# Kernel optimization log

Measured on AMD Instinct MI355X. Metric: run time of the kernel, lower is better.

## Reference

```python
import jax, jax.numpy as jnp
from jax import lax
import numpy as np

T, B, I, H, F, KEEP = 1000, 512, 64, 64, 128, 5
ALPHA = 20.0 / 100.0  # dt / tau


def setup_inputs() -> dict:
    key = jax.random.key(0)
    ks = jax.random.split(key, 9)
    s = 1.0 / np.sqrt(H)
    return {
        "x": jax.random.normal(ks[0], (T, B, I), jnp.float32),
        "h0": jnp.zeros((B, H), jnp.float32),
        "W_in": jax.random.normal(ks[1], (H, I), jnp.float32) * s,
        "b_in": jax.random.normal(ks[2], (H,), jnp.float32) * s,
        "W_hh": jax.random.normal(ks[3], (H, H), jnp.float32) * s,
        "b_hh": jax.random.normal(ks[4], (H,), jnp.float32) * s,
        "W1": jax.random.normal(ks[5], (F, KEEP * H), jnp.float32) / np.sqrt(KEEP * H),
        "b1": jax.random.normal(ks[6], (F,), jnp.float32) * 0.01,
        "W2": jax.random.normal(ks[7], (H, F), jnp.float32) / np.sqrt(F),
        "b2": jax.random.normal(ks[8], (H,), jnp.float32) * 0.01,
    }


def reference(x, h0, W_in, b_in, W_hh, b_hh, W1, b1, W2, b2):
    # CT-RNN with leaky integration; feedback via MLP on the last 5 hiddens
    # once 5 steps have accumulated. KC = 0.5*I, so the feedback mix is
    # h = 0.5*h_obs + 0.5*h_mlp.
    Tn, Bn, _ = x.shape
    Hn = h0.shape[1]
    buf0 = jnp.zeros((KEEP, Bn, Hn), x.dtype)  # oldest-first ring of hiddens

    def step(carry, inp):
        h, buf = carry
        xt, i = inp
        h_obs = jax.nn.relu(xt @ W_in.T + b_in + h @ W_hh.T + b_hh)
        h_obs = h * (1.0 - ALPHA) + h_obs * ALPHA
        # mlp feedback on concat of last 5 hiddens (oldest..newest) -> [B, 5H]
        mlp_in = buf.transpose(1, 0, 2).reshape(Bn, KEEP * Hn)
        h_mlp = jax.nn.relu(mlp_in @ W1.T + b1) @ W2.T + b2
        h_new = jnp.where(i >= KEEP, 0.5 * h_obs + 0.5 * h_mlp, h_obs)
        buf = jnp.concatenate([buf[1:], h_new[None]], axis=0)
        return (h_new, buf), h_new

    (hT, _), out = lax.scan(step, (h0, buf0), (x, jnp.arange(Tn)))
    return out, hT
```

## Files before the change

### kernel.cpp

```cpp
#include <hip/hip_runtime.h>

typedef short bf16x8 __attribute__((ext_vector_type(8)));
typedef float f32x4  __attribute__((ext_vector_type(4)));

#define TSTEPS 1000
#define BATCH  512
#define HID    64
#define INPD   64
#define FEAT   128
#define KEEP   5
#define KH     320
#define ALPHA  0.2f
#define BB     2
#define NBLK   (BATCH/BB)
#define NTHR   512

#define MFMA(a,b,c) __builtin_amdgcn_mfma_f32_16x16x32_bf16(a, b, c, 0, 0, 0)

template<int P> struct IC { static constexpr int v = P; };

__device__ __forceinline__ void barrier_fast() {
  asm volatile("s_waitcnt lgkmcnt(0)" ::: "memory");
  __builtin_amdgcn_s_barrier();
  asm volatile("" ::: "memory");
}

__device__ __forceinline__ float qx2(float v) {
  return __uint_as_float((unsigned)__builtin_amdgcn_update_dpp(
      0, (int)__float_as_uint(v), 0x4E , 0xF, 0xF, true));
}
__device__ __forceinline__ f32x4 fold2(f32x4 v) {
  f32x4 r;
  r.x = v.x + qx2(v.x);
  r.y = v.y + qx2(v.y);
  r.z = v.z + qx2(v.z);
  r.w = v.w + qx2(v.w);
  return r;
}

__device__ __forceinline__ void pack4(float x0, float x1, float x2, float x3,
                                      unsigned &h0, unsigned &h1,
                                      unsigned &l0, unsigned &l1) {
  unsigned a0 = __float_as_uint(x0), a1 = __float_as_uint(x1);
  unsigned a2 = __float_as_uint(x2), a3 = __float_as_uint(x3);
  h0 = __builtin_amdgcn_perm(a1, a0, 0x07060302u);
  h1 = __builtin_amdgcn_perm(a3, a2, 0x07060302u);
  float r0 = x0 - __uint_as_float(a0 & 0xFFFF0000u);
  float r1 = x1 - __uint_as_float(a1 & 0xFFFF0000u);
  float r2 = x2 - __uint_as_float(a2 & 0xFFFF0000u);
  float r3 = x3 - __uint_as_float(a3 & 0xFFFF0000u);
  asm("v_cvt_pk_bf16_f32 %0, %1, %2" : "=v"(l0) : "v"(r0), "v"(r1));
  asm("v_cvt_pk_bf16_f32 %0, %1, %2" : "=v"(l1) : "v"(r2), "v"(r3));
}

__device__ __forceinline__ void pack_frag(float4 v0, float4 v1, bf16x8 &hi, bf16x8 &lo) {
  int4 h4, l4;
  pack4(v0.x, v0.y, v0.z, v0.w, (unsigned&)h4.x, (unsigned&)h4.y, (unsigned&)l4.x, (unsigned&)l4.y);
  pack4(v1.x, v1.y, v1.z, v1.w, (unsigned&)h4.z, (unsigned&)h4.w, (unsigned&)l4.z, (unsigned&)l4.w);
  hi = __builtin_bit_cast(bf16x8, h4);
  lo = __builtin_bit_cast(bf16x8, l4);
}

__device__ __forceinline__ void load_wfrag(const float* p, bf16x8 &hi, bf16x8 &lo) {
  float4 v0 = *(const float4*)p;
  float4 v1 = *(const float4*)(p + 4);
  pack_frag(v0, v1, hi, lo);
}

__global__ __launch_bounds__(NTHR, 2) void seq_kernel(
    const float* __restrict__ x,    float* __restrict__ io,
    const float* __restrict__ h0g,
    const float* __restrict__ W_in, const float* __restrict__ b_in,
    const float* __restrict__ W_hh, const float* __restrict__ b_hh,
    const float* __restrict__ W1,   const float* __restrict__ b1,
    const float* __restrict__ W2,   const float* __restrict__ b2) {

  __shared__ __align__(16) short B1lds[1024];
  __shared__ __align__(16) short a_s[512];
  __shared__ __align__(16) float xin_s[2][128];

  const int tid  = threadIdx.x;
  const int w    = tid >> 6;
  const int lane = tid & 63;
  const int q15  = lane & 15;
  const int g    = lane >> 4;
  const int b0   = blockIdx.x * BB;
  const bool gA  = (w < 4);
  const int r0c  = 16*(w & 3) + 4*g;
  const int f0   = 16*w + 4*g;
  const int c01  = q15 & 1;

  const int aWH = (w>>1)*128 + (2*(w&1) + (g>>1))*32 + q15*8 + 4*(g&1);
  const int aRD = g*32 + (q15 & 3)*8;
  const int bWH = ((w&3)>>1)*512 + ((2*(w&3) + (g>>1)) & 3)*128 + q15*8 + 4*(g&1);
  const int bRD = g*128 + q15*8;

  const f32x4 vz = {0.f, 0.f, 0.f, 0.f};
  const bf16x8 z8 = {0,0,0,0,0,0,0,0};

  bf16x8 w1h[10], w1l[10];
#pragma unroll
  for (int jt = 0; jt < 10; ++jt)
    load_wfrag(W1 + (size_t)(16*w + q15)*KH + jt*32 + 8*g, w1h[jt], w1l[jt]);

  bf16x8 wxh[6], wxl[6];
#pragma unroll
  for (int i = 0; i < 6; ++i) { wxh[i] = z8; wxl[i] = z8; }
  f32x4 biasv = vz, b2r = vz;
  f32x4 b1r = *(const f32x4*)(b1 + f0);
  if (gA) {
#pragma unroll
    for (int kt = 0; kt < 2; ++kt)
      load_wfrag(W_hh + (size_t)(16*w + q15)*HID + kt*32 + 8*g, wxh[kt], wxl[kt]);
#pragma unroll
    for (int kt = 0; kt < 4; ++kt)
      load_wfrag(W2 + (size_t)(16*w + q15)*FEAT + kt*32 + 8*g, wxh[2+kt], wxl[2+kt]);
    b2r = *(const f32x4*)(b2 + r0c);
  } else {
#pragma unroll
    for (int kt = 0; kt < 2; ++kt)
      load_wfrag(W_in + (size_t)(16*(w-4) + q15)*INPD + kt*32 + 8*g, wxh[kt], wxl[kt]);
    biasv = *(const f32x4*)(b_in + r0c) + *(const f32x4*)(b_hh + r0c);
  }

  for (int i = tid; i < 512; i += NTHR) ((unsigned*)B1lds)[i] = 0u;
  __syncthreads();

  float* ioP = io + (size_t)(b0 + q15)*HID + r0c;
  float* ioF = io + (size_t)TSTEPS*BATCH*HID + (size_t)(b0 + q15)*HID + r0c;
  const float* xP = x + (size_t)2*BATCH*INPD + (size_t)(b0 + c01)*INPD + 8*g;

  f32x4 hprev = vz;
  float4 xc0, xc1, xc2, xc3;
  if (gA) {
    if (q15 < 2) {
      hprev = *(const f32x4*)(h0g + (size_t)(b0 + q15)*HID + r0c);
      unsigned n0, n1, n2, n3;
      pack4(hprev.x, hprev.y, hprev.z, hprev.w, n0, n1, n2, n3);
      *(uint2*)&B1lds[bWH]      = make_uint2(n0, n1);
      *(uint2*)&B1lds[bWH + 16] = make_uint2(n2, n3);
    }
  } else {
    const float* xp0 = x + (size_t)(b0 + c01)*INPD + 8*g;
    float4 v0 = *(const float4*)xp0;        float4 v1 = *(const float4*)(xp0 + 4);
    float4 v2 = *(const float4*)(xp0 + 32); float4 v3 = *(const float4*)(xp0 + 36);
    bf16x8 th0, tl0, th1, tl1;
    pack_frag(v0, v1, th0, tl0);
    pack_frag(v2, v3, th1, tl1);
    bf16x8 f0b = (q15 & 2) ? tl0 : th0;
    bf16x8 f1b = (q15 & 2) ? tl1 : th1;
    f32x4 aHx = MFMA(wxh[0], f0b, vz);
    f32x4 aLx = MFMA(wxl[0], f0b, vz);
    aHx = MFMA(wxh[1], f1b, aHx);
    aLx = MFMA(wxl[1], f1b, aLx);
    f32x4 xi = fold2(aHx + aLx) + biasv;
    if (q15 < 2) *(f32x4*)&xin_s[0][q15*64 + r0c] = xi;
    const float* xq = x + (size_t)1*BATCH*INPD + (size_t)(b0 + c01)*INPD + 8*g;
    xc0 = *(const float4*)xq;        xc1 = *(const float4*)(xq + 4);
    xc2 = *(const float4*)(xq + 32); xc3 = *(const float4*)(xq + 36);
  }

  bf16x8 rb[KEEP][2];
#pragma unroll
  for (int s = 0; s < KEEP; ++s) { rb[s][0] = z8; rb[s][1] = z8; }

  f32x4 accH = vz, accL = vz;
  __syncthreads();

  int t5 = 0;
  auto step = [&](auto pc) {
    constexpr int ph = decltype(pc)::v;
    constexpr int sN = (ph + 4) % 5;
    constexpr int s1 = (ph + 1) % 5;
    constexpr int s2 = (ph + 2) % 5;
    constexpr int s3 = (ph + 3) % 5;
    const int t = t5 + ph;

    rb[sN][0] = *(const bf16x8*)&B1lds[bRD];
    rb[sN][1] = *(const bf16x8*)&B1lds[bRD + 512];

    f32x4 tH = MFMA(w1h[9], rb[sN][1], vz);
    f32x4 tL = MFMA(w1l[9], rb[sN][1], vz);
    accH = MFMA(w1h[8], rb[sN][0], accH);
    accL = MFMA(w1l[8], rb[sN][0], accL);
    {
      f32x4 apre = fold2((accH + tH) + (accL + tL)) + b1r;
      f32x4 av = __builtin_elementwise_max(apre, vz);
      unsigned p0, p1, p2, p3;
      pack4(av.x, av.y, av.z, av.w, p0, p1, p2, p3);
      if (q15 < 2) {
        *(uint2*)&a_s[aWH]      = make_uint2(p0, p1);
        *(uint2*)&a_s[aWH + 16] = make_uint2(p2, p3);
      }
    }
    barrier_fast();

    f32x4 nHa, nHb, nLa, nLb;
    if (gA) {
      bf16x8 af0 = *(const bf16x8*)&a_s[aRD +   0];
      bf16x8 af1 = *(const bf16x8*)&a_s[aRD + 128];
      bf16x8 af2 = *(const bf16x8*)&a_s[aRD + 256];
      bf16x8 af3 = *(const bf16x8*)&a_s[aRD + 384];
      f32x4 xinv = *(const f32x4*)&xin_s[t & 1][(q15 & 1)*64 + r0c];
      nHa = MFMA(w1h[0], rb[s1][0], vz);
      nLa = MFMA(w1l[0], rb[s1][0], vz);
      nHb = MFMA(w1h[2], rb[s2][0], vz);
      nLb = MFMA(w1l[2], rb[s2][0], vz);
      nHa = MFMA(w1h[1], rb[s1][1], nHa);
      nLa = MFMA(w1l[1], rb[s1][1], nLa);
      nHb = MFMA(w1h[3], rb[s2][1], nHb);
      nLb = MFMA(w1l[3], rb[s2][1], nLb);
      nHa = MFMA(w1h[4], rb[s3][0], nHa);
      nLa = MFMA(w1l[4], rb[s3][0], nLa);
      nHb = MFMA(w1h[6], rb[sN][0], nHb);
      nLb = MFMA(w1l[6], rb[sN][0], nLb);
      nHa = MFMA(w1h[5], rb[s3][1], nHa);
      nLa = MFMA(w1l[5], rb[s3][1], nLa);
      nHb = MFMA(w1h[7], rb[sN][1], nHb);
      nLb = MFMA(w1l[7], rb[sN][1], nLb);
      f32x4 rH0 = MFMA(wxh[0], rb[sN][0], vz);
      f32x4 rL0 = MFMA(wxl[0], rb[sN][0], vz);
      f32x4 rH1 = MFMA(wxh[1], rb[sN][1], vz);
      f32x4 rL1 = MFMA(wxl[1], rb[sN][1], vz);
      f32x4 mH0 = MFMA(wxh[2], af0, vz);
      f32x4 mL0 = MFMA(wxl[2], af0, vz);
      f32x4 mH1 = MFMA(wxh[4], af2, vz);
      f32x4 mL1 = MFMA(wxl[4], af2, vz);
      mH0 = MFMA(wxh[3], af1, mH0);
      mL0 = MFMA(wxl[3], af1, mL0);
      mH1 = MFMA(wxh[5], af3, mH1);
      mL1 = MFMA(wxl[5], af3, mL1);
      f32x4 pre = fold2((rH0 + rH1) + (rL0 + rL1)) + xinv;
      f32x4 rl_ = __builtin_elementwise_max(pre, vz);
      f32x4 hobs = hprev * (1.f - ALPHA) + rl_ * ALPHA;
      f32x4 hm = fold2((mH0 + mH1) + (mL0 + mL1)) + b2r;
      f32x4 hn = (t >= KEEP) ? (hobs + hm) * 0.5f : hobs;
      if (q15 < 2) {
        *(f32x4*)ioP = hn;
        if (t == TSTEPS-1) *(f32x4*)ioF = hn;
        unsigned n0, n1, n2, n3;
        pack4(hn.x, hn.y, hn.z, hn.w, n0, n1, n2, n3);
        *(uint2*)&B1lds[bWH]      = make_uint2(n0, n1);
        *(uint2*)&B1lds[bWH + 16] = make_uint2(n2, n3);
      }
      hprev = hn;
    } else {
      float4 xn0 = *(const float4*)xP;        float4 xn1 = *(const float4*)(xP + 4);
      float4 xn2 = *(const float4*)(xP + 32); float4 xn3 = *(const float4*)(xP + 36);
      nHa = MFMA(w1h[0], rb[s1][0], vz);
      nLa = MFMA(w1l[0], rb[s1][0], vz);
      nHb = MFMA(w1h[2], rb[s2][0], vz);
      nLb = MFMA(w1l[2], rb[s2][0], vz);
      nHa = MFMA(w1h[1], rb[s1][1], nHa);
      nLa = MFMA(w1l[1], rb[s1][1], nLa);
      nHb = MFMA(w1h[3], rb[s2][1], nHb);
      nLb = MFMA(w1l[3], rb[s2][1], nLb);
      nHa = MFMA(w1h[4], rb[s3][0], nHa);
      nLa = MFMA(w1l[4], rb[s3][0], nLa);
      nHb = MFMA(w1h[6], rb[sN][0], nHb);
      nLb = MFMA(w1l[6], rb[sN][0], nLb);
      nHa = MFMA(w1h[5], rb[s3][1], nHa);
      nLa = MFMA(w1l[5], rb[s3][1], nLa);
      nHb = MFMA(w1h[7], rb[sN][1], nHb);
      nLb = MFMA(w1l[7], rb[sN][1], nLb);
      bf16x8 th0, tl0, th1, tl1;
      pack_frag(xc0, xc1, th0, tl0);
      pack_frag(xc2, xc3, th1, tl1);
      bf16x8 f0b = (q15 & 2) ? tl0 : th0;
      bf16x8 f1b = (q15 & 2) ? tl1 : th1;
      f32x4 xH0 = MFMA(wxh[0], f0b, vz);
      f32x4 xL0 = MFMA(wxl[0], f0b, vz);
      f32x4 xH1 = MFMA(wxh[1], f1b, vz);
      f32x4 xL1 = MFMA(wxl[1], f1b, vz);
      f32x4 xi = fold2((xH0 + xH1) + (xL0 + xL1)) + biasv;
      if (q15 < 2) *(f32x4*)&xin_s[(t + 1) & 1][q15*64 + r0c] = xi;
      xc0 = xn0; xc1 = xn1; xc2 = xn2; xc3 = xn3;
      if (t < TSTEPS-3) xP += BATCH*INPD;
    }
    accH = nHa + nHb;
    accL = nLa + nLb;
    ioP += BATCH*HID;
    barrier_fast();
  };

  for (t5 = 0; t5 < TSTEPS; t5 += 5) {
    step(IC<0>{});
    step(IC<1>{});
    step(IC<2>{});
    step(IC<3>{});
    step(IC<4>{});
  }
}

extern "C" void kernel_launch(void* const* d_in, const int* in_sizes, int n_in,
                              void* d_out, int out_size, void* d_ws, size_t ws_size,
                              hipStream_t stream) {
  (void)in_sizes; (void)n_in; (void)out_size; (void)d_ws; (void)ws_size;
  const float* x    = (const float*)d_in[0];
  const float* h0   = (const float*)d_in[1];
  const float* W_in = (const float*)d_in[2];
  const float* b_in = (const float*)d_in[3];
  const float* W_hh = (const float*)d_in[4];
  const float* b_hh = (const float*)d_in[5];
  const float* W1   = (const float*)d_in[6];
  const float* b1   = (const float*)d_in[7];
  const float* W2   = (const float*)d_in[8];
  const float* b2   = (const float*)d_in[9];
  float* out = (float*)d_out;

  seq_kernel<<<NBLK, NTHR, 0, stream>>>(x, out, h0, W_in, b_in, W_hh, b_hh, W1, b1, W2, b2);
}
```

Measured before the change: 927.7 us.

## Rebalance MFMA work between warp groups across the mid-step barrier

Result: slower. 1.018 ms (+9.8%).

```diff
diff --git a/kernel.cpp b/kernel.cpp
--- a/kernel.cpp
+++ b/kernel.cpp
@@ -179,11 +179,11 @@
     rb[sN][0] = *(const bf16x8*)&B1lds[bRD];
     rb[sN][1] = *(const bf16x8*)&B1lds[bRD + 512];
 
-    f32x4 tH = MFMA(w1h[9], rb[sN][1], vz);
-    f32x4 tL = MFMA(w1l[9], rb[sN][1], vz);
-    accH = MFMA(w1h[8], rb[sN][0], accH);
-    accL = MFMA(w1l[8], rb[sN][0], accL);
-    {
+    if (gA) {
+      f32x4 tH = MFMA(w1h[9], rb[sN][1], vz);
+      f32x4 tL = MFMA(w1l[9], rb[sN][1], vz);
+      accH = MFMA(w1h[8], rb[sN][0], accH);
+      accL = MFMA(w1l[8], rb[sN][0], accL);
       f32x4 apre = fold2((accH + tH) + (accL + tL)) + b1r;
       f32x4 av = __builtin_elementwise_max(apre, vz);
       unsigned p0, p1, p2, p3;
@@ -192,20 +192,63 @@
         *(uint2*)&a_s[aWH]      = make_uint2(p0, p1);
         *(uint2*)&a_s[aWH + 16] = make_uint2(p2, p3);
       }
+    } else {
+      f32x4 nHa = MFMA(w1h[0], rb[s1][0], vz);
+      f32x4 nLa = MFMA(w1l[0], rb[s1][0], vz);
+      f32x4 nHb = MFMA(w1h[2], rb[s2][0], vz);
+      f32x4 nLb = MFMA(w1l[2], rb[s2][0], vz);
+      nHa = MFMA(w1h[1], rb[s1][1], nHa);
+      nLa = MFMA(w1l[1], rb[s1][1], nLa);
+      nHb = MFMA(w1h[3], rb[s2][1], nHb);
+      nLb = MFMA(w1l[3], rb[s2][1], nLb);
+      nHa = MFMA(w1h[4], rb[s3][0], nHa);
+      nLa = MFMA(w1l[4], rb[s3][0], nLa);
+      nHa = MFMA(w1h[5], rb[s3][1], nHa);
+      nLa = MFMA(w1l[5], rb[s3][1], nLa);
+      f32x4 tH = MFMA(w1h[9], rb[sN][1], vz);
+      f32x4 tL = MFMA(w1l[9], rb[sN][1], vz);
+      accH = MFMA(w1h[8], rb[sN][0], accH);
+      accL = MFMA(w1l[8], rb[sN][0], accL);
+      {
+        f32x4 apre = fold2((accH + tH) + (accL + tL)) + b1r;
+        f32x4 av = __builtin_elementwise_max(apre, vz);
+        unsigned p0, p1, p2, p3;
+        pack4(av.x, av.y, av.z, av.w, p0, p1, p2, p3);
+        if (q15 < 2) {
+          *(uint2*)&a_s[aWH]      = make_uint2(p0, p1);
+          *(uint2*)&a_s[aWH + 16] = make_uint2(p2, p3);
+        }
+      }
+      nHb = MFMA(w1h[6], rb[sN][0], nHb);
+      nLb = MFMA(w1l[6], rb[sN][0], nLb);
+      nHb = MFMA(w1h[7], rb[sN][1], nHb);
+      nLb = MFMA(w1l[7], rb[sN][1], nLb);
+      bf16x8 th0, tl0, th1, tl1;
+      pack_frag(xc0, xc1, th0, tl0);
+      pack_frag(xc2, xc3, th1, tl1);
+      bf16x8 f0b = (q15 & 2) ? tl0 : th0;
+      bf16x8 f1b = (q15 & 2) ? tl1 : th1;
+      f32x4 xH0 = MFMA(wxh[0], f0b, vz);
+      f32x4 xL0 = MFMA(wxl[0], f0b, vz);
+      f32x4 xH1 = MFMA(wxh[1], f1b, vz);
+      f32x4 xL1 = MFMA(wxl[1], f1b, vz);
+      f32x4 xi = fold2((xH0 + xH1) + (xL0 + xL1)) + biasv;
+      if (q15 < 2) *(f32x4*)&xin_s[(t + 1) & 1][q15*64 + r0c] = xi;
+      accH = nHa + nHb;
+      accL = nLa + nLb;
     }
     barrier_fast();
 
-    f32x4 nHa, nHb, nLa, nLb;
     if (gA) {
       bf16x8 af0 = *(const bf16x8*)&a_s[aRD +   0];
       bf16x8 af1 = *(const bf16x8*)&a_s[aRD + 128];
       bf16x8 af2 = *(const bf16x8*)&a_s[aRD + 256];
       bf16x8 af3 = *(const bf16x8*)&a_s[aRD + 384];
       f32x4 xinv = *(const f32x4*)&xin_s[t & 1][(q15 & 1)*64 + r0c];
-      nHa = MFMA(w1h[0], rb[s1][0], vz);
-      nLa = MFMA(w1l[0], rb[s1][0], vz);
-      nHb = MFMA(w1h[2], rb[s2][0], vz);
-      nLb = MFMA(w1l[2], rb[s2][0], vz);
+      f32x4 nHa = MFMA(w1h[0], rb[s1][0], vz);
+      f32x4 nLa = MFMA(w1l[0], rb[s1][0], vz);
+      f32x4 nHb = MFMA(w1h[2], rb[s2][0], vz);
+      f32x4 nLb = MFMA(w1l[2], rb[s2][0], vz);
       nHa = MFMA(w1h[1], rb[s1][1], nHa);
       nLa = MFMA(w1l[1], rb[s1][1], nLa);
       nHb = MFMA(w1h[3], rb[s2][1], nHb);
@@ -244,41 +287,13 @@
         *(uint2*)&B1lds[bWH + 16] = make_uint2(n2, n3);
       }
       hprev = hn;
+      accH = nHa + nHb;
+      accL = nLa + nLb;
     } else {
-      float4 xn0 = *(const float4*)xP;        float4 xn1 = *(const float4*)(xP + 4);
-      float4 xn2 = *(const float4*)(xP + 32); float4 xn3 = *(const float4*)(xP + 36);
-      nHa = MFMA(w1h[0], rb[s1][0], vz);
-      nLa = MFMA(w1l[0], rb[s1][0], vz);
-      nHb = MFMA(w1h[2], rb[s2][0], vz);
-      nLb = MFMA(w1l[2], rb[s2][0], vz);
-      nHa = MFMA(w1h[1], rb[s1][1], nHa);
-      nLa = MFMA(w1l[1], rb[s1][1], nLa);
-      nHb = MFMA(w1h[3], rb[s2][1], nHb);
-      nLb = MFMA(w1l[3], rb[s2][1], nLb);
-      nHa = MFMA(w1h[4], rb[s3][0], nHa);
-      nLa = MFMA(w1l[4], rb[s3][0], nLa);
-      nHb = MFMA(w1h[6], rb[sN][0], nHb);
-      nLb = MFMA(w1l[6], rb[sN][0], nLb);
-      nHa = MFMA(w1h[5], rb[s3][1], nHa);
-      nLa = MFMA(w1l[5], rb[s3][1], nLa);
-      nHb = MFMA(w1h[7], rb[sN][1], nHb);
-      nLb = MFMA(w1l[7], rb[sN][1], nLb);
-      bf16x8 th0, tl0, th1, tl1;
-      pack_frag(xc0, xc1, th0, tl0);
-      pack_frag(xc2, xc3, th1, tl1);
-      bf16x8 f0b = (q15 & 2) ? tl0 : th0;
-      bf16x8 f1b = (q15 & 2) ? tl1 : th1;
-      f32x4 xH0 = MFMA(wxh[0], f0b, vz);
-      f32x4 xL0 = MFMA(wxl[0], f0b, vz);
-      f32x4 xH1 = MFMA(wxh[1], f1b, vz);
-      f32x4 xL1 = MFMA(wxl[1], f1b, vz);
-      f32x4 xi = fold2((xH0 + xH1) + (xL0 + xL1)) + biasv;
-      if (q15 < 2) *(f32x4*)&xin_s[(t + 1) & 1][q15*64 + r0c] = xi;
-      xc0 = xn0; xc1 = xn1; xc2 = xn2; xc3 = xn3;
+      xc0 = *(const float4*)xP;        xc1 = *(const float4*)(xP + 4);
+      xc2 = *(const float4*)(xP + 32); xc3 = *(const float4*)(xP + 36);
       if (t < TSTEPS-3) xP += BATCH*INPD;
     }
-    accH = nHa + nHb;
-    accL = nLa + nLb;
     ioP += BATCH*HID;
     barrier_fast();
   };
```
